# Optimization experiments

Measured on AMD Instinct MI355X. Metric: run time of the kernel, lower is better.

The kernel has to match this reference:

```python
import jax, jax.numpy as jnp
import numpy as np
import math

B, SL, CH, HZ = 128, 5000, 12, 100
L, D, DFF, H, NC = 5, 1024, 4096, 16, 71
NI = CH * HZ  # 1200
S = SL // HZ  # 50


def setup_inputs() -> dict:
    key = jax.random.key(0)
    ks = jax.random.split(key, 12)
    r = lambda k, shp, sc: jax.random.normal(k, shp, jnp.float32) * sc
    return {
        'x': r(ks[0], (B, SL, CH), 1.0),
        'embed_w': r(ks[1], (NI, D), NI ** -0.5),
        'attn_w': r(ks[2], (L, 4, D, D), D ** -0.5),
        'attn_b': r(ks[3], (L, 4, D), 0.01),
        'ff_w1': r(ks[4], (L, D, DFF), D ** -0.5),
        'ff_b1': r(ks[5], (L, DFF), 0.01),
        'ff_w2': r(ks[6], (L, DFF, D), DFF ** -0.5),
        'ff_b2': r(ks[7], (L, D), 0.01),
        'ln_g': jnp.ones((L, 2, D)), 'ln_b': jnp.zeros((L, 2, D)),
        'fin_g': jnp.ones((D,)), 'fin_b': jnp.zeros((D,)),
        'cf_bn_g': jnp.ones((D,)), 'cf_bn_b': jnp.zeros((D,)),
        'cf_w': r(ks[8], (D, D), D ** -0.5), 'cf_b': r(ks[9], (D,), 0.01),
        'fc_bn_g': jnp.ones((D,)), 'fc_bn_b': jnp.zeros((D,)),
        'fc_w': r(ks[10], (D, NC), D ** -0.5), 'fc_b': r(ks[11], (NC,), 0.01),
    }


def _ln(t, g, b, eps=1e-6):
    # torch LayerNorm variant in source: unbiased std (ddof=1), divide by (std + eps)
    m = t.mean(-1, keepdims=True)
    s = jnp.std(t, axis=-1, ddof=1, keepdims=True)
    return g * (t - m) / (s + eps) + b


def reference(x, embed_w, attn_w, attn_b, ff_w1, ff_b1, ff_w2, ff_b2,
              ln_g, ln_b, fin_g, fin_b, cf_bn_g, cf_bn_b, cf_w, cf_b,
              fc_bn_g, fc_bn_b, fc_w, fc_b):
    Bx, SLx, CHx = x.shape
    Sx = SLx // HZ
    Dx = embed_w.shape[1]
    dk = Dx // H
    # Segmentation (fix): [B, SL, CH] -> [B, S, CH*HZ]; input embed (no bias)
    h = x.reshape(Bx, Sx, CHx * HZ) @ embed_w
    # Positional encoding (sin/cos, detached buffer)
    pos = jnp.arange(Sx, dtype=jnp.float32)[:, None]
    div = jnp.exp(jnp.arange(0, Dx, 2, dtype=jnp.float32) * (-math.log(10000.0) / Dx))
    pe = jnp.zeros((Sx, Dx), jnp.float32)
    pe = pe.at[:, 0::2].set(jnp.sin(pos * div)).at[:, 1::2].set(jnp.cos(pos * div))
    h = h + pe[None]
    # Pre-norm encoder stack (dropout = identity in eval)
    for i in range(attn_w.shape[0]):
        a = _ln(h, ln_g[i, 0], ln_b[i, 0])
        qkv = jnp.einsum('bsd,kde->kbse', a, attn_w[i, :3]) + attn_b[i, :3][:, None, None, :]
        q, k, v = [t.reshape(Bx, Sx, H, dk).transpose(0, 2, 1, 3) for t in qkv]  # bhsd
        sc = jnp.einsum('bhqd,bhkd->bhqk', q, k) / math.sqrt(dk)
        p = jax.nn.softmax(sc, axis=-1)
        o = jnp.einsum('bhqk,bhkd->bhqd', p, v).transpose(0, 2, 1, 3).reshape(Bx, Sx, Dx)
        h = h + o @ attn_w[i, 3] + attn_b[i, 3]
        a2 = _ln(h, ln_g[i, 1], ln_b[i, 1])
        h = h + jax.nn.relu(a2 @ ff_w1[i] + ff_b1[i]) @ ff_w2[i] + ff_b2[i]
    h = _ln(h, fin_g, fin_b)
    # LastPoolRNN(bidirectional=False): last time step
    pooled = h[:, -1, :]
    # BatchNorm1d in eval with running_mean=0, running_var=1
    inv = 1.0 / math.sqrt(1.0 + 1e-5)
    z = (pooled * inv) * cf_bn_g + cf_bn_b
    z = jax.nn.relu(z @ cf_w + cf_b)
    z = (z * inv) * fc_bn_g + fc_bn_b
    return z @ fc_w + fc_b
```

## Files before the change

kernel.cpp:

```cpp
#include <hip/hip_runtime.h>
#include <hip/hip_bf16.h>


typedef __attribute__((ext_vector_type(4))) float f32x4;
typedef __attribute__((ext_vector_type(8))) __bf16 bfvec8;

#define MTOT 6400
#define DMODEL 1024
#define KEMB 1216

__device__ __forceinline__ unsigned short f2bf(float x) {
    __hip_bfloat16 t = __float2bfloat16(x);
    return *reinterpret_cast<unsigned short*>(&t);
}

__device__ __forceinline__ void gl2lds16(const void* g, void* l) {
    __builtin_amdgcn_global_load_lds(
        (__attribute__((address_space(1))) void*)(g),
        (__attribute__((address_space(3))) void*)(l), 16, 0, 0);
}

__global__ __launch_bounds__(256) void tconv(const float* __restrict__ W,
                                             __hip_bfloat16* __restrict__ Wt,
                                             int K, int N, int Kpad, size_t zoff) {
    __shared__ float t[32][33];
    const float* Wz = W + (size_t)blockIdx.z * zoff;
    unsigned short* Wtz = (unsigned short*)Wt + (size_t)blockIdx.z * zoff;
    const int n0 = blockIdx.x * 32, k0 = blockIdx.y * 32;
    const int tx = threadIdx.x, ty = threadIdx.y;
#pragma unroll
    for (int j = 0; j < 4; ++j) {
        int k = k0 + ty + j * 8, n = n0 + tx;
        float v = (k < K && n < N) ? Wz[(size_t)k * N + n] : 0.f;
        t[ty + j * 8][tx] = v;
    }
    __syncthreads();
#pragma unroll
    for (int j = 0; j < 4; ++j) {
        int n = n0 + ty + j * 8, k = k0 + tx;
        if (n < N && k < Kpad)
            Wtz[(size_t)n * Kpad + k] = f2bf(t[tx][ty + j * 8]);
    }
}

__global__ __launch_bounds__(256) void xconv(const float* __restrict__ x,
                                             __hip_bfloat16* __restrict__ xb) {
    int q = blockIdx.x * 256 + threadIdx.x;
    if (q >= MTOT * (KEMB / 4)) return;
    int m = q / (KEMB / 4), kq = q - m * (KEMB / 4);
    ushort4 o;
    if (kq < 300) {
        float4 v = reinterpret_cast<const float4*>(x + (size_t)m * 1200)[kq];
        o.x = f2bf(v.x); o.y = f2bf(v.y); o.z = f2bf(v.z); o.w = f2bf(v.w);
    } else { o.x = 0; o.y = 0; o.z = 0; o.w = 0; }
    reinterpret_cast<ushort4*>(xb)[q] = o;
}

__global__ __launch_bounds__(256) void pe_kernel(float* __restrict__ pe) {
    int idx = blockIdx.x * 256 + threadIdx.x;
    if (idx >= 50 * 512) return;
    int s = idx >> 9, i = idx & 511;
    float dv = expf((float)(2 * i) * (-9.210340371976184f / 1024.0f));
    float a = (float)s * dv;
    pe[(s << 10) + 2 * i] = sinf(a);
    pe[(s << 10) + 2 * i + 1] = cosf(a);
}

template<int FLAGS>
__global__ __launch_bounds__(256) void gemm_bt(
                        const __hip_bfloat16* __restrict__ A,
                        const __hip_bfloat16* __restrict__ Bt,
                        float* __restrict__ outF, __hip_bfloat16* __restrict__ outB,
                        const float* __restrict__ bias, const float* __restrict__ res,
                        const float* __restrict__ pe,
                        const float* __restrict__ psg, const float* __restrict__ psb,
                        int M, int N, int K) {
    __shared__ short lds[16384];
    const int tid = threadIdx.x;
    const int w = tid >> 6, l = tid & 63;

    int bx, by;
    {
        const int nwg = gridDim.x * gridDim.y;
        const int wg  = blockIdx.y * gridDim.x + blockIdx.x;
        const int q = nwg >> 3, r = nwg & 7;
        const int xcd = wg & 7, pos = wg >> 3;
        const int nid = (xcd < r) ? xcd * (q + 1) + pos
                                  : r * (q + 1) + (xcd - r) * q + pos;
        by = nid / gridDim.x;
        bx = nid - by * gridDim.x;
    }
    const int row0 = by * 128, col0 = bx * 128;
    const int l15 = l & 15, kof = (l >> 4) << 3;
    const int wr = (w >> 1) << 6, wc = (w & 1) << 6;

    f32x4 acc[4][4];
#pragma unroll
    for (int m = 0; m < 4; ++m)
#pragma unroll
        for (int n = 0; n < 4; ++n) acc[m][n] = (f32x4){0.f, 0.f, 0.f, 0.f};

    int sr[4], sc[4];
#pragma unroll
    for (int c = 0; c < 4; ++c) {
        int e = c * 2048 + w * 512 + l * 8;
        int r = e >> 6;
        int cb = (e & 63) << 1;
        sr[c] = r;
        sc[c] = (cb ^ ((r & 7) << 4)) >> 1;
    }
    const int swz = (l15 & 7) << 4;

    for (int k0 = 0; k0 < K; k0 += 64) {
#pragma unroll
        for (int c = 0; c < 4; ++c)
            gl2lds16(A + (size_t)(row0 + sr[c]) * K + (k0 + sc[c]),
                     &lds[c * 2048 + w * 512]);
#pragma unroll
        for (int c = 0; c < 4; ++c)
            gl2lds16(Bt + (size_t)(col0 + sr[c]) * K + (k0 + sc[c]),
                     &lds[8192 + c * 2048 + w * 512]);
        __syncthreads();
#pragma unroll
        for (int kk = 0; kk < 64; kk += 32) {
            bfvec8 af[4], bfr[4];
#pragma unroll
            for (int m = 0; m < 4; ++m) {
                int r = wr + m * 16 + l15;
                af[m] = *(const bfvec8*)((const char*)lds + r * 128 + ((((kk + kof) << 1)) ^ swz));
            }
#pragma unroll
            for (int n = 0; n < 4; ++n) {
                int r = wc + n * 16 + l15;
                bfr[n] = *(const bfvec8*)((const char*)lds + 16384 + r * 128 + ((((kk + kof) << 1)) ^ swz));
            }
#pragma unroll
            for (int m = 0; m < 4; ++m)
#pragma unroll
                for (int n = 0; n < 4; ++n)
                    acc[m][n] = __builtin_amdgcn_mfma_f32_16x16x32_bf16(af[m], bfr[n], acc[m][n], 0, 0, 0);
        }
        __syncthreads();
    }

    const int rb = row0 + wr + ((l >> 4) << 2);
#pragma unroll
    for (int n = 0; n < 4; ++n) {
        const int cidx = col0 + wc + n * 16 + l15;
        float bv = 0.f, pg = 0.f, pb2 = 0.f;
        if constexpr (FLAGS & 1) bv = bias[cidx];
        if constexpr (FLAGS & 16) {
            pg = 0.99999500003749971f * psg[cidx];
            pb2 = psb[cidx];
        }
#pragma unroll
        for (int m = 0; m < 4; ++m) {
#pragma unroll
            for (int i = 0; i < 4; ++i) {
                int r = rb + m * 16 + i;
                float v = acc[m][n][i] + bv;
                if constexpr (FLAGS & 8) v += pe[(r % 50) * N + cidx];
                if constexpr (FLAGS & 4) v = fmaxf(v, 0.f);
                if constexpr (FLAGS & 2) v += res[(size_t)r * N + cidx];
                if constexpr (FLAGS & 16) v = v * pg + pb2;
                if constexpr (FLAGS & 32) ((unsigned short*)outB)[(size_t)r * N + cidx] = f2bf(v);
                else outF[(size_t)r * N + cidx] = v;
            }
        }
    }
}

__device__ __forceinline__ float wave_sum(float v) {
#pragma unroll
    for (int off = 32; off; off >>= 1) v += __shfl_down(v, off);
    return v;
}

__global__ __launch_bounds__(256) void ln_kernel(const float* __restrict__ h,
                                                 const float* __restrict__ g,
                                                 const float* __restrict__ b,
                                                 __hip_bfloat16* __restrict__ out) {
    const int row = blockIdx.x, tid = threadIdx.x;
    const float4 v = reinterpret_cast<const float4*>(h + (size_t)row * 1024)[tid];
    float s = v.x + v.y + v.z + v.w;
    float s2 = v.x * v.x + v.y * v.y + v.z * v.z + v.w * v.w;
    __shared__ float red[8];
    float ws1 = wave_sum(s), ws2 = wave_sum(s2);
    if ((tid & 63) == 0) { red[tid >> 6] = ws1; red[4 + (tid >> 6)] = ws2; }
    __syncthreads();
    float sum = red[0] + red[1] + red[2] + red[3];
    float sum2 = red[4] + red[5] + red[6] + red[7];
    float mean = sum * (1.f / 1024.f);
    float var = fmaxf(0.f, (sum2 - sum * mean) * (1.f / 1023.f));
    float inv = 1.f / (sqrtf(var) + 1e-6f);
    float4 gv = reinterpret_cast<const float4*>(g)[tid];
    float4 bv = reinterpret_cast<const float4*>(b)[tid];
    ushort4 o;
    o.x = f2bf(gv.x * (v.x - mean) * inv + bv.x);
    o.y = f2bf(gv.y * (v.y - mean) * inv + bv.y);
    o.z = f2bf(gv.z * (v.z - mean) * inv + bv.z);
    o.w = f2bf(gv.w * (v.w - mean) * inv + bv.w);
    reinterpret_cast<ushort4*>(out)[(size_t)row * 256 + tid] = o;
}

__global__ __launch_bounds__(128) void attn_mfma(const __hip_bfloat16* __restrict__ qkv,
                                                 __hip_bfloat16* __restrict__ o) {
    __shared__ unsigned short plds[2][64 * 72];
    __shared__ unsigned short vlds[2][64 * 72];
    const int w = threadIdx.x >> 6, l = threadIdx.x & 63;
    const int b = blockIdx.x >> 3;
    const int hh = ((blockIdx.x & 7) << 1) | w;
    const int l15 = l & 15, g = l >> 4;
    const size_t rowbase = (size_t)(b * 50) * 3072 + hh * 64;

    {
        const int j = l;
        const bool ok = j < 50;
        const uint4* vp = (const uint4*)(qkv + rowbase + (size_t)j * 3072 + 2048);
#pragma unroll
        for (int d8 = 0; d8 < 8; ++d8) {
            uint4 vv = ok ? vp[d8] : (uint4){0u, 0u, 0u, 0u};
            const int d0 = d8 * 8;
            vlds[w][(d0 + 0) * 72 + j] = (unsigned short)(vv.x & 0xffff);
            vlds[w][(d0 + 1) * 72 + j] = (unsigned short)(vv.x >> 16);
            vlds[w][(d0 + 2) * 72 + j] = (unsigned short)(vv.y & 0xffff);
            vlds[w][(d0 + 3) * 72 + j] = (unsigned short)(vv.y >> 16);
            vlds[w][(d0 + 4) * 72 + j] = (unsigned short)(vv.z & 0xffff);
            vlds[w][(d0 + 5) * 72 + j] = (unsigned short)(vv.z >> 16);
            vlds[w][(d0 + 6) * 72 + j] = (unsigned short)(vv.w & 0xffff);
            vlds[w][(d0 + 7) * 72 + j] = (unsigned short)(vv.w >> 16);
        }
    }

    const bfvec8 zf = {};
    bfvec8 qf[4][2], kf[4][2];
#pragma unroll
    for (int mi = 0; mi < 4; ++mi) {
        const int i = mi * 16 + l15;
        const bool ok = i < 50;
        const size_t rq = rowbase + (size_t)i * 3072;
#pragma unroll
        for (int ks = 0; ks < 2; ++ks) {
            const int d = ks * 32 + g * 8;
            qf[mi][ks] = ok ? *(const bfvec8*)(qkv + rq + d) : zf;
            kf[mi][ks] = ok ? *(const bfvec8*)(qkv + rq + 1024 + d) : zf;
        }
    }

    f32x4 s[4][4];
#pragma unroll
    for (int mi = 0; mi < 4; ++mi)
#pragma unroll
        for (int nj = 0; nj < 4; ++nj) {
            s[mi][nj] = (f32x4){0.f, 0.f, 0.f, 0.f};
#pragma unroll
            for (int ks = 0; ks < 2; ++ks)
                s[mi][nj] = __builtin_amdgcn_mfma_f32_16x16x32_bf16(qf[mi][ks], kf[nj][ks], s[mi][nj], 0, 0, 0);
        }

#pragma unroll
    for (int mi = 0; mi < 4; ++mi) {
#pragma unroll
        for (int r = 0; r < 4; ++r) {
            const int row = mi * 16 + g * 4 + r;
            float v[4];
            float mx = -1e30f;
#pragma unroll
            for (int nj = 0; nj < 4; ++nj) {
                float x = s[mi][nj][r] * 0.125f;
                if (nj * 16 + l15 >= 50) x = -1e30f;
                v[nj] = x;
                mx = fmaxf(mx, x);
            }
#pragma unroll
            for (int m = 1; m < 16; m <<= 1) mx = fmaxf(mx, __shfl_xor(mx, m));
            float sum = 0.f;
#pragma unroll
            for (int nj = 0; nj < 4; ++nj) { v[nj] = __expf(v[nj] - mx); sum += v[nj]; }
#pragma unroll
            for (int m = 1; m < 16; m <<= 1) sum += __shfl_xor(sum, m);
            const float is = 1.f / sum;
#pragma unroll
            for (int nj = 0; nj < 4; ++nj)
                plds[w][row * 72 + nj * 16 + l15] = f2bf(v[nj] * is);
        }
    }
    __syncthreads();

    bfvec8 pa[4][2], vb[4][2];
#pragma unroll
    for (int mi = 0; mi < 4; ++mi)
#pragma unroll
        for (int ks = 0; ks < 2; ++ks)
            pa[mi][ks] = *(const bfvec8*)(plds[w] + (mi * 16 + l15) * 72 + ks * 32 + g * 8);
#pragma unroll
    for (int dn = 0; dn < 4; ++dn)
#pragma unroll
        for (int ks = 0; ks < 2; ++ks)
            vb[dn][ks] = *(const bfvec8*)(vlds[w] + (dn * 16 + l15) * 72 + ks * 32 + g * 8);

    f32x4 oa[4][4];
#pragma unroll
    for (int mi = 0; mi < 4; ++mi)
#pragma unroll
        for (int dn = 0; dn < 4; ++dn) {
            oa[mi][dn] = (f32x4){0.f, 0.f, 0.f, 0.f};
#pragma unroll
            for (int ks = 0; ks < 2; ++ks)
                oa[mi][dn] = __builtin_amdgcn_mfma_f32_16x16x32_bf16(pa[mi][ks], vb[dn][ks], oa[mi][dn], 0, 0, 0);
        }

#pragma unroll
    for (int mi = 0; mi < 4; ++mi) {
#pragma unroll
        for (int r = 0; r < 4; ++r) {
            const int i = mi * 16 + g * 4 + r;
            if (i < 50) {
                const size_t ob = (size_t)(b * 50 + i) * 1024 + hh * 64;
#pragma unroll
                for (int dn = 0; dn < 4; ++dn)
                    ((unsigned short*)o)[ob + dn * 16 + l15] = f2bf(oa[mi][dn][r]);
            }
        }
    }
}

__global__ __launch_bounds__(256) void pool_kernel(const float* __restrict__ h,
                                                   const float* __restrict__ fg,
                                                   const float* __restrict__ fb,
                                                   const float* __restrict__ cg,
                                                   const float* __restrict__ cb,
                                                   __hip_bfloat16* __restrict__ z) {
    const int bb = blockIdx.x, tid = threadIdx.x;
    const size_t row = (size_t)bb * 50 + 49;
    const float4 v = reinterpret_cast<const float4*>(h + row * 1024)[tid];
    float s = v.x + v.y + v.z + v.w;
    float s2 = v.x * v.x + v.y * v.y + v.z * v.z + v.w * v.w;
    __shared__ float red[8];
    float ws1 = wave_sum(s), ws2 = wave_sum(s2);
    if ((tid & 63) == 0) { red[tid >> 6] = ws1; red[4 + (tid >> 6)] = ws2; }
    __syncthreads();
    float sum = red[0] + red[1] + red[2] + red[3];
    float sum2 = red[4] + red[5] + red[6] + red[7];
    float mean = sum * (1.f / 1024.f);
    float var = fmaxf(0.f, (sum2 - sum * mean) * (1.f / 1023.f));
    float inv = 1.f / (sqrtf(var) + 1e-6f);
    const float INV = 0.99999500003749971f;
    float4 gv = reinterpret_cast<const float4*>(fg)[tid];
    float4 bv = reinterpret_cast<const float4*>(fb)[tid];
    float4 cgv = reinterpret_cast<const float4*>(cg)[tid];
    float4 cbv = reinterpret_cast<const float4*>(cb)[tid];
    ushort4 o;
    o.x = f2bf((gv.x * (v.x - mean) * inv + bv.x) * INV * cgv.x + cbv.x);
    o.y = f2bf((gv.y * (v.y - mean) * inv + bv.y) * INV * cgv.y + cbv.y);
    o.z = f2bf((gv.z * (v.z - mean) * inv + bv.z) * INV * cgv.z + cbv.z);
    o.w = f2bf((gv.w * (v.w - mean) * inv + bv.w) * INV * cgv.w + cbv.w);
    reinterpret_cast<ushort4*>(z)[(size_t)bb * 256 + tid] = o;
}

__global__ __launch_bounds__(128) void fc_kernel(const __hip_bfloat16* __restrict__ z3,
                                                 const float* __restrict__ fw,
                                                 const float* __restrict__ fbias,
                                                 float* __restrict__ out) {
    __shared__ float zr[1024];
    const int b = blockIdx.x, tid = threadIdx.x;
    for (int i = tid; i < 1024; i += 128) zr[i] = __bfloat162float(z3[(size_t)b * 1024 + i]);
    __syncthreads();
    if (tid < 71) {
        float acc = 0.f;
        for (int k = 0; k < 1024; ++k) acc += zr[k] * fw[k * 71 + tid];
        out[b * 71 + tid] = acc + fbias[tid];
    }
}

extern "C" void kernel_launch(void* const* d_in, const int* in_sizes, int n_in,
                              void* d_out, int out_size, void* d_ws, size_t ws_size,
                              hipStream_t stream) {
    const float* x       = (const float*)d_in[0];
    const float* embed_w = (const float*)d_in[1];
    const float* attn_w  = (const float*)d_in[2];
    const float* attn_b  = (const float*)d_in[3];
    const float* ff_w1   = (const float*)d_in[4];
    const float* ff_b1   = (const float*)d_in[5];
    const float* ff_w2   = (const float*)d_in[6];
    const float* ff_b2   = (const float*)d_in[7];
    const float* ln_g    = (const float*)d_in[8];
    const float* ln_b    = (const float*)d_in[9];
    const float* fin_g   = (const float*)d_in[10];
    const float* fin_b   = (const float*)d_in[11];
    const float* cf_bn_g = (const float*)d_in[12];
    const float* cf_bn_b = (const float*)d_in[13];
    const float* cf_w    = (const float*)d_in[14];
    const float* cf_b    = (const float*)d_in[15];
    const float* fc_bn_g = (const float*)d_in[16];
    const float* fc_bn_b = (const float*)d_in[17];
    const float* fc_w    = (const float*)d_in[18];
    const float* fc_b    = (const float*)d_in[19];

    char* ws = (char*)d_ws;
    size_t off = 0;
    auto alloc = [&](size_t bytes) { void* p = ws + off; off += (bytes + 255) & ~(size_t)255; return p; };

    __hip_bfloat16* wbuf = (__hip_bfloat16*)alloc((size_t)12582912 * 2);
    float*          h    = (float*)alloc((size_t)MTOT * DMODEL * 4);
    __hip_bfloat16* abuf = (__hip_bfloat16*)alloc((size_t)MTOT * DMODEL * 2);
    __hip_bfloat16* big  = (__hip_bfloat16*)alloc((size_t)MTOT * 4096 * 2);
    float*          pe   = (float*)alloc((size_t)50 * 1024 * 4);
    __hip_bfloat16* zbuf = (__hip_bfloat16*)alloc((size_t)128 * 1024 * 2);
    __hip_bfloat16* z3   = (__hip_bfloat16*)alloc((size_t)128 * 1024 * 2);

    __hip_bfloat16* qkvT = wbuf;
    __hip_bfloat16* ff1T = wbuf + (size_t)4096 * 1024;
    __hip_bfloat16* ff2T = wbuf + (size_t)8192 * 1024;
    __hip_bfloat16* projT = wbuf + (size_t)3072 * 1024;

    const dim3 tb(32, 8);

    xconv<<<(MTOT * (KEMB / 4) + 255) / 256, 256, 0, stream>>>(x, big);
    pe_kernel<<<100, 256, 0, stream>>>(pe);
    tconv<<<dim3(32, 38), tb, 0, stream>>>(embed_w, wbuf, 1200, 1024, KEMB, 0);
    gemm_bt<8><<<dim3(8, 50), 256, 0, stream>>>(big, wbuf, h, nullptr,
        nullptr, nullptr, pe, nullptr, nullptr, MTOT, DMODEL, KEMB);

    for (int i = 0; i < 5; ++i) {
        tconv<<<dim3(32, 32, 4), tb, 0, stream>>>(attn_w + (size_t)i * 4194304,
                                                  qkvT, 1024, 1024, 1024, 1048576);
        tconv<<<dim3(128, 32), tb, 0, stream>>>(ff_w1 + (size_t)i * 4194304, ff1T, 1024, 4096, 1024, 0);
        tconv<<<dim3(32, 128), tb, 0, stream>>>(ff_w2 + (size_t)i * 4194304, ff2T, 4096, 1024, 4096, 0);

        ln_kernel<<<MTOT, 256, 0, stream>>>(h, ln_g + (size_t)i * 2048, ln_b + (size_t)i * 2048, abuf);
        gemm_bt<33><<<dim3(24, 50), 256, 0, stream>>>(abuf, qkvT, nullptr, big,
            attn_b + (size_t)i * 4096, nullptr, nullptr, nullptr, nullptr, MTOT, 3072, 1024);
        attn_mfma<<<1024, 128, 0, stream>>>(big, abuf);
        gemm_bt<3><<<dim3(8, 50), 256, 0, stream>>>(abuf, projT, h, nullptr,
            attn_b + (size_t)i * 4096 + 3072, h, nullptr, nullptr, nullptr, MTOT, DMODEL, 1024);
        ln_kernel<<<MTOT, 256, 0, stream>>>(h, ln_g + (size_t)i * 2048 + 1024,
                                            ln_b + (size_t)i * 2048 + 1024, abuf);
        gemm_bt<37><<<dim3(32, 50), 256, 0, stream>>>(abuf, ff1T, nullptr, big,
            ff_b1 + (size_t)i * 4096, nullptr, nullptr, nullptr, nullptr, MTOT, 4096, 1024);
        gemm_bt<3><<<dim3(8, 50), 256, 0, stream>>>(big, ff2T, h, nullptr,
            ff_b2 + (size_t)i * 1024, h, nullptr, nullptr, nullptr, MTOT, DMODEL, 4096);
    }

    pool_kernel<<<128, 256, 0, stream>>>(h, fin_g, fin_b, cf_bn_g, cf_bn_b, zbuf);
    tconv<<<dim3(32, 32), tb, 0, stream>>>(cf_w, wbuf, 1024, 1024, 1024, 0);
    gemm_bt<53><<<dim3(8, 1), 256, 0, stream>>>(zbuf, wbuf, nullptr, z3,
        cf_b, nullptr, nullptr, fc_bn_g, fc_bn_b, 128, 1024, 1024);
    fc_kernel<<<128, 128, 0, stream>>>(z3, fc_w, fc_b, (float*)d_out);

    (void)in_sizes; (void)n_in; (void)out_size; (void)ws_size;
}
```

Before: 1.895 ms.

## Double-buffer GEMM LDS with BK=32 and persistent tile loop for FF1

Rewrites the bf16 GEMM main loop to use two LDS buffers with K-step 32, issuing the next tile's global-to-LDS loads before computing the current one and waiting with partial vmcnt. This overlaps memory and MFMA work instead of serialising load, sync and compute. A 1D grid-stride persistent tile loop also lets the FF1 GEMM run 1280 blocks over 1600 tiles, prefetching across tile boundaries. The smaller K-step doubles barrier count per K, and the new swizzle changes the LDS bank pattern.

```diff
diff --git a/kernel.cpp b/kernel.cpp
--- a/kernel.cpp
+++ b/kernel.cpp
@@ -74,25 +74,45 @@
                         const float* __restrict__ bias, const float* __restrict__ res,
                         const float* __restrict__ pe,
                         const float* __restrict__ psg, const float* __restrict__ psb,
-                        int M, int N, int K) {
-    __shared__ short lds[16384];
+                        int M, int N, int K, int gx, int T) {
+    __shared__ short lds[2][8192];
     const int tid = threadIdx.x;
     const int w = tid >> 6, l = tid & 63;
-
-    int bx, by;
-    {
-        const int nwg = gridDim.x * gridDim.y;
-        const int wg  = blockIdx.y * gridDim.x + blockIdx.x;
-        const int q = nwg >> 3, r = nwg & 7;
-        const int xcd = wg & 7, pos = wg >> 3;
-        const int nid = (xcd < r) ? xcd * (q + 1) + pos
-                                  : r * (q + 1) + (xcd - r) * q + pos;
-        by = nid / gridDim.x;
-        bx = nid - by * gridDim.x;
-    }
-    const int row0 = by * 128, col0 = bx * 128;
-    const int l15 = l & 15, kof = (l >> 4) << 3;
+    const int l15 = l & 15, g = l >> 4;
     const int wr = (w >> 1) << 6, wc = (w & 1) << 6;
+    const int G = gridDim.x;
+
+    int sr[2], sc[2];
+#pragma unroll
+    for (int c = 0; c < 2; ++c) {
+        int e = c * 2048 + tid * 8;
+        int r = e >> 5;
+        int cb = (e & 31) << 1;
+        sr[c] = r;
+        sc[c] = (cb ^ (((r >> 1) & 3) << 4)) >> 1;
+    }
+    const int rdxor = ((l15 >> 1) & 3) << 4;
+
+    auto MAP = [&](int t, int& r0, int& c0) {
+        const int q = T >> 3, rr = T & 7;
+        const int xcd = t & 7, pos = t >> 3;
+        const int nid = (xcd < rr) ? xcd * (q + 1) + pos
+                                   : rr * (q + 1) + (xcd - rr) * q + pos;
+        const int by = nid / gx;
+        r0 = by * 128;
+        c0 = (nid - by * gx) * 128;
+    };
+
+    auto STAGE = [&](int slot, int r0, int c0, int k0) {
+#pragma unroll
+        for (int c = 0; c < 2; ++c)
+            gl2lds16(A + (size_t)(r0 + sr[c]) * K + (k0 + sc[c]),
+                     &lds[slot][c * 2048 + w * 512]);
+#pragma unroll
+        for (int c = 0; c < 2; ++c)
+            gl2lds16(Bt + (size_t)(c0 + sr[c]) * K + (k0 + sc[c]),
+                     &lds[slot][4096 + c * 2048 + w * 512]);
+    };
 
     f32x4 acc[4][4];
 #pragma unroll
@@ -100,73 +120,84 @@
 #pragma unroll
         for (int n = 0; n < 4; ++n) acc[m][n] = (f32x4){0.f, 0.f, 0.f, 0.f};
 
-    int sr[4], sc[4];
-#pragma unroll
-    for (int c = 0; c < 4; ++c) {
-        int e = c * 2048 + w * 512 + l * 8;
-        int r = e >> 6;
-        int cb = (e & 63) << 1;
-        sr[c] = r;
-        sc[c] = (cb ^ ((r & 7) << 4)) >> 1;
-    }
-    const int swz = (l15 & 7) << 4;
-
-    for (int k0 = 0; k0 < K; k0 += 64) {
-#pragma unroll
-        for (int c = 0; c < 4; ++c)
-            gl2lds16(A + (size_t)(row0 + sr[c]) * K + (k0 + sc[c]),
-                     &lds[c * 2048 + w * 512]);
-#pragma unroll
-        for (int c = 0; c < 4; ++c)
-            gl2lds16(Bt + (size_t)(col0 + sr[c]) * K + (k0 + sc[c]),
-                     &lds[8192 + c * 2048 + w * 512]);
-        __syncthreads();
-#pragma unroll
-        for (int kk = 0; kk < 64; kk += 32) {
-            bfvec8 af[4], bfr[4];
+    int t_lin = blockIdx.x;
+    if (t_lin >= T) return;
+    int row0, col0;
+    MAP(t_lin, row0, col0);
+
+    STAGE(0, row0, col0, 0);
+    int cur = 0, k0 = 0;
+
+    for (;;) {
+        int nrow0 = row0, ncol0 = col0, nk0 = k0 + 32, nt_lin = t_lin;
+        bool have_next = true;
+        if (nk0 == K) {
+            nt_lin = t_lin + G;
+            if (nt_lin < T) { MAP(nt_lin, nrow0, ncol0); nk0 = 0; }
+            else have_next = false;
+        }
+        if (have_next) {
+            STAGE(cur ^ 1, nrow0, ncol0, nk0);
+            asm volatile("s_waitcnt vmcnt(4)" ::: "memory");
+        } else {
+            asm volatile("s_waitcnt vmcnt(0)" ::: "memory");
+        }
+        __builtin_amdgcn_s_barrier();
+        __builtin_amdgcn_sched_barrier(0);
+
+        {
+            bfvec8 af[4], bf[4];
+            const char* base = (const char*)lds[cur];
+#pragma unroll
+            for (int m = 0; m < 4; ++m)
+                af[m] = *(const bfvec8*)(base + (wr + m * 16 + l15) * 64 + ((g * 16) ^ rdxor));
+#pragma unroll
+            for (int n = 0; n < 4; ++n)
+                bf[n] = *(const bfvec8*)(base + 8192 + (wc + n * 16 + l15) * 64 + ((g * 16) ^ rdxor));
+#pragma unroll
+            for (int m = 0; m < 4; ++m)
+#pragma unroll
+                for (int n = 0; n < 4; ++n)
+                    acc[m][n] = __builtin_amdgcn_mfma_f32_16x16x32_bf16(af[m], bf[n], acc[m][n], 0, 0, 0);
+        }
+        __builtin_amdgcn_sched_barrier(0);
+        __builtin_amdgcn_s_barrier();
+        __builtin_amdgcn_sched_barrier(0);
+        cur ^= 1;
+
+        if (nk0 != 0 && have_next) { k0 = nk0; continue; }
+
+        const int rb = row0 + wr + (g << 2);
+#pragma unroll
+        for (int n = 0; n < 4; ++n) {
+            const int cidx = col0 + wc + n * 16 + l15;
+            float bv = 0.f, pg = 0.f, pb2 = 0.f;
+            if constexpr (FLAGS & 1) bv = bias[cidx];
+            if constexpr (FLAGS & 16) {
+                pg = 0.99999500003749971f * psg[cidx];
+                pb2 = psb[cidx];
+            }
 #pragma unroll
             for (int m = 0; m < 4; ++m) {
-                int r = wr + m * 16 + l15;
-                af[m] = *(const bfvec8*)((const char*)lds + r * 128 + ((((kk + kof) << 1)) ^ swz));
+#pragma unroll
+                for (int i = 0; i < 4; ++i) {
+                    int r = rb + m * 16 + i;
+                    float v = acc[m][n][i] + bv;
+                    if constexpr (FLAGS & 8) v += pe[(r % 50) * N + cidx];
+                    if constexpr (FLAGS & 4) v = fmaxf(v, 0.f);
+                    if constexpr (FLAGS & 2) v += res[(size_t)r * N + cidx];
+                    if constexpr (FLAGS & 16) v = v * pg + pb2;
+                    if constexpr (FLAGS & 32) ((unsigned short*)outB)[(size_t)r * N + cidx] = f2bf(v);
+                    else outF[(size_t)r * N + cidx] = v;
+                }
             }
-#pragma unroll
-            for (int n = 0; n < 4; ++n) {
-                int r = wc + n * 16 + l15;
-                bfr[n] = *(const bfvec8*)((const char*)lds + 16384 + r * 128 + ((((kk + kof) << 1)) ^ swz));
-            }
-#pragma unroll
-            for (int m = 0; m < 4; ++m)
-#pragma unroll
-                for (int n = 0; n < 4; ++n)
-                    acc[m][n] = __builtin_amdgcn_mfma_f32_16x16x32_bf16(af[m], bfr[n], acc[m][n], 0, 0, 0);
-        }
-        __syncthreads();
-    }
-
-    const int rb = row0 + wr + ((l >> 4) << 2);
-#pragma unroll
-    for (int n = 0; n < 4; ++n) {
-        const int cidx = col0 + wc + n * 16 + l15;
-        float bv = 0.f, pg = 0.f, pb2 = 0.f;
-        if constexpr (FLAGS & 1) bv = bias[cidx];
-        if constexpr (FLAGS & 16) {
-            pg = 0.99999500003749971f * psg[cidx];
-            pb2 = psb[cidx];
-        }
-#pragma unroll
-        for (int m = 0; m < 4; ++m) {
-#pragma unroll
-            for (int i = 0; i < 4; ++i) {
-                int r = rb + m * 16 + i;
-                float v = acc[m][n][i] + bv;
-                if constexpr (FLAGS & 8) v += pe[(r % 50) * N + cidx];
-                if constexpr (FLAGS & 4) v = fmaxf(v, 0.f);
-                if constexpr (FLAGS & 2) v += res[(size_t)r * N + cidx];
-                if constexpr (FLAGS & 16) v = v * pg + pb2;
-                if constexpr (FLAGS & 32) ((unsigned short*)outB)[(size_t)r * N + cidx] = f2bf(v);
-                else outF[(size_t)r * N + cidx] = v;
-            }
-        }
+        }
+        if (!have_next) break;
+#pragma unroll
+        for (int m = 0; m < 4; ++m)
+#pragma unroll
+            for (int n = 0; n < 4; ++n) acc[m][n] = (f32x4){0.f, 0.f, 0.f, 0.f};
+        t_lin = nt_lin; row0 = nrow0; col0 = ncol0; k0 = 0;
     }
 }
 
@@ -419,8 +450,8 @@
     xconv<<<(MTOT * (KEMB / 4) + 255) / 256, 256, 0, stream>>>(x, big);
     pe_kernel<<<100, 256, 0, stream>>>(pe);
     tconv<<<dim3(32, 38), tb, 0, stream>>>(embed_w, wbuf, 1200, 1024, KEMB, 0);
-    gemm_bt<8><<<dim3(8, 50), 256, 0, stream>>>(big, wbuf, h, nullptr,
-        nullptr, nullptr, pe, nullptr, nullptr, MTOT, DMODEL, KEMB);
+    gemm_bt<8><<<400, 256, 0, stream>>>(big, wbuf, h, nullptr,
+        nullptr, nullptr, pe, nullptr, nullptr, MTOT, DMODEL, KEMB, 8, 400);
 
     for (int i = 0; i < 5; ++i) {
         tconv<<<dim3(32, 32, 4), tb, 0, stream>>>(attn_w + (size_t)i * 4194304,
@@ -429,23 +460,23 @@
         tconv<<<dim3(32, 128), tb, 0, stream>>>(ff_w2 + (size_t)i * 4194304, ff2T, 4096, 1024, 4096, 0);
 
         ln_kernel<<<MTOT, 256, 0, stream>>>(h, ln_g + (size_t)i * 2048, ln_b + (size_t)i * 2048, abuf);
-        gemm_bt<33><<<dim3(24, 50), 256, 0, stream>>>(abuf, qkvT, nullptr, big,
-            attn_b + (size_t)i * 4096, nullptr, nullptr, nullptr, nullptr, MTOT, 3072, 1024);
+        gemm_bt<33><<<1200, 256, 0, stream>>>(abuf, qkvT, nullptr, big,
+            attn_b + (size_t)i * 4096, nullptr, nullptr, nullptr, nullptr, MTOT, 3072, 1024, 24, 1200);
         attn_mfma<<<1024, 128, 0, stream>>>(big, abuf);
-        gemm_bt<3><<<dim3(8, 50), 256, 0, stream>>>(abuf, projT, h, nullptr,
-            attn_b + (size_t)i * 4096 + 3072, h, nullptr, nullptr, nullptr, MTOT, DMODEL, 1024);
+        gemm_bt<3><<<400, 256, 0, stream>>>(abuf, projT, h, nullptr,
+            attn_b + (size_t)i * 4096 + 3072, h, nullptr, nullptr, nullptr, MTOT, DMODEL, 1024, 8, 400);
         ln_kernel<<<MTOT, 256, 0, stream>>>(h, ln_g + (size_t)i * 2048 + 1024,
                                             ln_b + (size_t)i * 2048 + 1024, abuf);
-        gemm_bt<37><<<dim3(32, 50), 256, 0, stream>>>(abuf, ff1T, nullptr, big,
-            ff_b1 + (size_t)i * 4096, nullptr, nullptr, nullptr, nullptr, MTOT, 4096, 1024);
-        gemm_bt<3><<<dim3(8, 50), 256, 0, stream>>>(big, ff2T, h, nullptr,
-            ff_b2 + (size_t)i * 1024, h, nullptr, nullptr, nullptr, MTOT, DMODEL, 4096);
+        gemm_bt<37><<<1280, 256, 0, stream>>>(abuf, ff1T, nullptr, big,
+            ff_b1 + (size_t)i * 4096, nullptr, nullptr, nullptr, nullptr, MTOT, 4096, 1024, 32, 1600);
+        gemm_bt<3><<<400, 256, 0, stream>>>(big, ff2T, h, nullptr,
+            ff_b2 + (size_t)i * 1024, h, nullptr, nullptr, nullptr, MTOT, DMODEL, 4096, 8, 400);
     }
 
     pool_kernel<<<128, 256, 0, stream>>>(h, fin_g, fin_b, cf_bn_g, cf_bn_b, zbuf);
     tconv<<<dim3(32, 32), tb, 0, stream>>>(cf_w, wbuf, 1024, 1024, 1024, 0);
-    gemm_bt<53><<<dim3(8, 1), 256, 0, stream>>>(zbuf, wbuf, nullptr, z3,
-        cf_b, nullptr, nullptr, fc_bn_g, fc_bn_b, 128, 1024, 1024);
+    gemm_bt<53><<<8, 256, 0, stream>>>(zbuf, wbuf, nullptr, z3,
+        cf_b, nullptr, nullptr, fc_bn_g, fc_bn_b, 128, 1024, 1024, 8, 8);
     fc_kernel<<<128, 128, 0, stream>>>(z3, fc_w, fc_b, (float*)d_out);
 
     (void)in_sizes; (void)n_in; (void)out_size; (void)ws_size;
```

After: 2.184 ms. 15.3% more time.

## Split-K the N=1024 residual GEMMs with atomic accumulation and fuse weight transposes

Applied to the files above, without the earlier changes.

The attention output projection and FF2 GEMMs, which only have 400 tiles, are now split along K (2 and 4 ways) and accumulate into the residual buffer h with float atomicAdd. This removes the separate residual read and raises the tile count to fill more CUs. The three per-layer weight transpose launches are merged into one kernel, and the K loop length becomes a template constant so it can be fully unrolled. In exchange, atomic adds cost extra memory traffic, the summation order becomes nondeterministic, and unrolling may raise code size and register pressure.

```diff
diff --git a/kernel.cpp b/kernel.cpp
--- a/kernel.cpp
+++ b/kernel.cpp
@@ -20,26 +20,53 @@
         (__attribute__((address_space(3))) void*)(l), 16, 0, 0);
 }
 
+__device__ __forceinline__ void tconv_tile(const float* __restrict__ W,
+                                           unsigned short* __restrict__ Wt,
+                                           int N, int Kpad, int n0, int k0,
+                                           int K, bool guard) {
+    __shared__ float t[32][33];
+    const int tx = threadIdx.x, ty = threadIdx.y;
+#pragma unroll
+    for (int j = 0; j < 4; ++j) {
+        int k = k0 + ty + j * 8, n = n0 + tx;
+        float v = (!guard || (k < K && n < N)) ? W[(size_t)k * N + n] : 0.f;
+        t[ty + j * 8][tx] = v;
+    }
+    __syncthreads();
+#pragma unroll
+    for (int j = 0; j < 4; ++j) {
+        int n = n0 + ty + j * 8, k = k0 + tx;
+        if (!guard || (n < N && k < Kpad))
+            Wt[(size_t)n * Kpad + k] = f2bf(t[tx][ty + j * 8]);
+    }
+}
+
 __global__ __launch_bounds__(256) void tconv(const float* __restrict__ W,
                                              __hip_bfloat16* __restrict__ Wt,
-                                             int K, int N, int Kpad, size_t zoff) {
-    __shared__ float t[32][33];
-    const float* Wz = W + (size_t)blockIdx.z * zoff;
-    unsigned short* Wtz = (unsigned short*)Wt + (size_t)blockIdx.z * zoff;
-    const int n0 = blockIdx.x * 32, k0 = blockIdx.y * 32;
-    const int tx = threadIdx.x, ty = threadIdx.y;
-#pragma unroll
-    for (int j = 0; j < 4; ++j) {
-        int k = k0 + ty + j * 8, n = n0 + tx;
-        float v = (k < K && n < N) ? Wz[(size_t)k * N + n] : 0.f;
-        t[ty + j * 8][tx] = v;
-    }
-    __syncthreads();
-#pragma unroll
-    for (int j = 0; j < 4; ++j) {
-        int n = n0 + ty + j * 8, k = k0 + tx;
-        if (n < N && k < Kpad)
-            Wtz[(size_t)n * Kpad + k] = f2bf(t[tx][ty + j * 8]);
+                                             int K, int N, int Kpad) {
+    tconv_tile(W, (unsigned short*)Wt, N, Kpad, blockIdx.x * 32, blockIdx.y * 32, K, true);
+}
+
+__global__ __launch_bounds__(256) void tconv_layer(const float* __restrict__ attn_w,
+                                                   const float* __restrict__ ff_w1,
+                                                   const float* __restrict__ ff_w2,
+                                                   __hip_bfloat16* __restrict__ qkvT,
+                                                   __hip_bfloat16* __restrict__ ff1T,
+                                                   __hip_bfloat16* __restrict__ ff2T) {
+    const int idx = blockIdx.x;
+    if (idx < 4096) {
+        const int z = idx >> 10, t = idx & 1023;
+        tconv_tile(attn_w + (size_t)z * 1048576,
+                   (unsigned short*)qkvT + (size_t)z * 1048576,
+                   1024, 1024, (t & 31) * 32, (t >> 5) * 32, 1024, false);
+    } else if (idx < 8192) {
+        const int t = idx - 4096;
+        tconv_tile(ff_w1, (unsigned short*)ff1T,
+                   4096, 1024, (t & 127) * 32, (t >> 7) * 32, 1024, false);
+    } else {
+        const int t = idx - 8192;
+        tconv_tile(ff_w2, (unsigned short*)ff2T,
+                   1024, 4096, (t & 31) * 32, (t >> 5) * 32, 4096, false);
     }
 }
 
@@ -66,7 +93,7 @@
     pe[(s << 10) + 2 * i + 1] = cosf(a);
 }
 
-template<int FLAGS>
+template<int FLAGS, int KT>
 __global__ __launch_bounds__(256) void gemm_bt(
                         const __hip_bfloat16* __restrict__ A,
                         const __hip_bfloat16* __restrict__ Bt,
@@ -74,7 +101,7 @@
                         const float* __restrict__ bias, const float* __restrict__ res,
                         const float* __restrict__ pe,
                         const float* __restrict__ psg, const float* __restrict__ psb,
-                        int M, int N, int K) {
+                        int M, int N, int SK) {
     __shared__ short lds[16384];
     const int tid = threadIdx.x;
     const int w = tid >> 6, l = tid & 63;
@@ -91,6 +118,7 @@
         bx = nid - by * gridDim.x;
     }
     const int row0 = by * 128, col0 = bx * 128;
+    const int kbase = blockIdx.z * KT;
     const int l15 = l & 15, kof = (l >> 4) << 3;
     const int wr = (w >> 1) << 6, wc = (w & 1) << 6;
 
@@ -111,14 +139,18 @@
     }
     const int swz = (l15 & 7) << 4;
 
-    for (int k0 = 0; k0 < K; k0 += 64) {
+    const __hip_bfloat16* Ab = A + (size_t)row0 * SK + kbase;
+    const __hip_bfloat16* Bb = Bt + (size_t)col0 * SK + kbase;
+
+#pragma unroll
+    for (int k0 = 0; k0 < KT; k0 += 64) {
 #pragma unroll
         for (int c = 0; c < 4; ++c)
-            gl2lds16(A + (size_t)(row0 + sr[c]) * K + (k0 + sc[c]),
+            gl2lds16(Ab + (size_t)sr[c] * SK + (k0 + sc[c]),
                      &lds[c * 2048 + w * 512]);
 #pragma unroll
         for (int c = 0; c < 4; ++c)
-            gl2lds16(Bt + (size_t)(col0 + sr[c]) * K + (k0 + sc[c]),
+            gl2lds16(Bb + (size_t)sr[c] * SK + (k0 + sc[c]),
                      &lds[8192 + c * 2048 + w * 512]);
         __syncthreads();
 #pragma unroll
@@ -148,7 +180,10 @@
     for (int n = 0; n < 4; ++n) {
         const int cidx = col0 + wc + n * 16 + l15;
         float bv = 0.f, pg = 0.f, pb2 = 0.f;
-        if constexpr (FLAGS & 1) bv = bias[cidx];
+        if constexpr (FLAGS & 1) {
+            if constexpr (FLAGS & 64) { if (blockIdx.z == 0) bv = bias[cidx]; }
+            else bv = bias[cidx];
+        }
         if constexpr (FLAGS & 16) {
             pg = 0.99999500003749971f * psg[cidx];
             pb2 = psb[cidx];
@@ -161,10 +196,14 @@
                 float v = acc[m][n][i] + bv;
                 if constexpr (FLAGS & 8) v += pe[(r % 50) * N + cidx];
                 if constexpr (FLAGS & 4) v = fmaxf(v, 0.f);
-                if constexpr (FLAGS & 2) v += res[(size_t)r * N + cidx];
-                if constexpr (FLAGS & 16) v = v * pg + pb2;
-                if constexpr (FLAGS & 32) ((unsigned short*)outB)[(size_t)r * N + cidx] = f2bf(v);
-                else outF[(size_t)r * N + cidx] = v;
+                if constexpr (FLAGS & 64) {
+                    atomicAdd(&outF[(size_t)r * N + cidx], v);
+                } else {
+                    if constexpr (FLAGS & 2) v += res[(size_t)r * N + cidx];
+                    if constexpr (FLAGS & 16) v = v * pg + pb2;
+                    if constexpr (FLAGS & 32) ((unsigned short*)outB)[(size_t)r * N + cidx] = f2bf(v);
+                    else outF[(size_t)r * N + cidx] = v;
+                }
             }
         }
     }
@@ -410,41 +449,41 @@
     __hip_bfloat16* z3   = (__hip_bfloat16*)alloc((size_t)128 * 1024 * 2);
 
     __hip_bfloat16* qkvT = wbuf;
+    __hip_bfloat16* projT = wbuf + (size_t)3072 * 1024;
     __hip_bfloat16* ff1T = wbuf + (size_t)4096 * 1024;
     __hip_bfloat16* ff2T = wbuf + (size_t)8192 * 1024;
-    __hip_bfloat16* projT = wbuf + (size_t)3072 * 1024;
 
     const dim3 tb(32, 8);
 
     xconv<<<(MTOT * (KEMB / 4) + 255) / 256, 256, 0, stream>>>(x, big);
     pe_kernel<<<100, 256, 0, stream>>>(pe);
-    tconv<<<dim3(32, 38), tb, 0, stream>>>(embed_w, wbuf, 1200, 1024, KEMB, 0);
-    gemm_bt<8><<<dim3(8, 50), 256, 0, stream>>>(big, wbuf, h, nullptr,
+    tconv<<<dim3(32, 38), tb, 0, stream>>>(embed_w, wbuf, 1200, 1024, KEMB);
+    gemm_bt<8, KEMB><<<dim3(8, 50), 256, 0, stream>>>(big, wbuf, h, nullptr,
         nullptr, nullptr, pe, nullptr, nullptr, MTOT, DMODEL, KEMB);
 
     for (int i = 0; i < 5; ++i) {
-        tconv<<<dim3(32, 32, 4), tb, 0, stream>>>(attn_w + (size_t)i * 4194304,
-                                                  qkvT, 1024, 1024, 1024, 1048576);
-        tconv<<<dim3(128, 32), tb, 0, stream>>>(ff_w1 + (size_t)i * 4194304, ff1T, 1024, 4096, 1024, 0);
-        tconv<<<dim3(32, 128), tb, 0, stream>>>(ff_w2 + (size_t)i * 4194304, ff2T, 4096, 1024, 4096, 0);
+        tconv_layer<<<12288, tb, 0, stream>>>(attn_w + (size_t)i * 4194304,
+                                              ff_w1 + (size_t)i * 4194304,
+                                              ff_w2 + (size_t)i * 4194304,
+                                              qkvT, ff1T, ff2T);
 
         ln_kernel<<<MTOT, 256, 0, stream>>>(h, ln_g + (size_t)i * 2048, ln_b + (size_t)i * 2048, abuf);
-        gemm_bt<33><<<dim3(24, 50), 256, 0, stream>>>(abuf, qkvT, nullptr, big,
+        gemm_bt<33, 1024><<<dim3(24, 50), 256, 0, stream>>>(abuf, qkvT, nullptr, big,
             attn_b + (size_t)i * 4096, nullptr, nullptr, nullptr, nullptr, MTOT, 3072, 1024);
         attn_mfma<<<1024, 128, 0, stream>>>(big, abuf);
-        gemm_bt<3><<<dim3(8, 50), 256, 0, stream>>>(abuf, projT, h, nullptr,
-            attn_b + (size_t)i * 4096 + 3072, h, nullptr, nullptr, nullptr, MTOT, DMODEL, 1024);
+        gemm_bt<65, 512><<<dim3(8, 50, 2), 256, 0, stream>>>(abuf, projT, h, nullptr,
+            attn_b + (size_t)i * 4096 + 3072, nullptr, nullptr, nullptr, nullptr, MTOT, DMODEL, 1024);
         ln_kernel<<<MTOT, 256, 0, stream>>>(h, ln_g + (size_t)i * 2048 + 1024,
                                             ln_b + (size_t)i * 2048 + 1024, abuf);
-        gemm_bt<37><<<dim3(32, 50), 256, 0, stream>>>(abuf, ff1T, nullptr, big,
+        gemm_bt<37, 1024><<<dim3(32, 50), 256, 0, stream>>>(abuf, ff1T, nullptr, big,
             ff_b1 + (size_t)i * 4096, nullptr, nullptr, nullptr, nullptr, MTOT, 4096, 1024);
-        gemm_bt<3><<<dim3(8, 50), 256, 0, stream>>>(big, ff2T, h, nullptr,
-            ff_b2 + (size_t)i * 1024, h, nullptr, nullptr, nullptr, MTOT, DMODEL, 4096);
+        gemm_bt<65, 1024><<<dim3(8, 50, 4), 256, 0, stream>>>(big, ff2T, h, nullptr,
+            ff_b2 + (size_t)i * 1024, nullptr, nullptr, nullptr, nullptr, MTOT, DMODEL, 4096);
     }
 
     pool_kernel<<<128, 256, 0, stream>>>(h, fin_g, fin_b, cf_bn_g, cf_bn_b, zbuf);
-    tconv<<<dim3(32, 32), tb, 0, stream>>>(cf_w, wbuf, 1024, 1024, 1024, 0);
-    gemm_bt<53><<<dim3(8, 1), 256, 0, stream>>>(zbuf, wbuf, nullptr, z3,
+    tconv<<<dim3(32, 32), tb, 0, stream>>>(cf_w, wbuf, 1024, 1024, 1024);
+    gemm_bt<53, 1024><<<dim3(8, 1), 256, 0, stream>>>(zbuf, wbuf, nullptr, z3,
         cf_b, nullptr, nullptr, fc_bn_g, fc_bn_b, 128, 1024, 1024);
     fc_kernel<<<128, 128, 0, stream>>>(z3, fc_w, fc_b, (float*)d_out);
 
```

Measured after the change: 2.109 ms. 1.11x slower.
